# Performance work log

Hardware: AMD Instinct MI355X
Metric: run time of the kernel (lower is better)

## Reference

```python
import jax, jax.numpy as jnp
import numpy as np

DIM = 1024
NUM_HEADS = 16
HEAD_DIM = DIM // NUM_HEADS
EPS = 1e-6


def setup_inputs() -> dict:
    key = jax.random.key(0)
    ks = jax.random.split(key, 9)
    B, S = 4, 4096
    std = 1.0 / np.sqrt(DIM)
    inp = {
        "x": jax.random.normal(ks[0], (B, S, DIM), dtype=jnp.float32),
        "attention_mask": jnp.ones((B, S), dtype=jnp.float32),
        "Wq": jax.random.normal(ks[1], (DIM, DIM), dtype=jnp.float32) * std,
        "bq": jnp.zeros((DIM,), dtype=jnp.float32),
        "Wk": jax.random.normal(ks[2], (DIM, DIM), dtype=jnp.float32) * std,
        "bk": jnp.zeros((DIM,), dtype=jnp.float32),
        "Wv": jax.random.normal(ks[3], (DIM, DIM), dtype=jnp.float32) * std,
        "bv": jnp.zeros((DIM,), dtype=jnp.float32),
        "Wo": jax.random.normal(ks[4], (DIM, DIM), dtype=jnp.float32) * std,
        "bo": jnp.zeros((DIM,), dtype=jnp.float32),
    }
    return inp


def _phi(x):
    # ELU + 1 feature map (positive-valued kernel features)
    return jax.nn.elu(x) + 1.0


def reference(x, attention_mask, Wq, bq, Wk, bk, Wv, bv, Wo, bo):
    B, S, _ = x.shape
    H, D = NUM_HEADS, HEAD_DIM
    q = (x @ Wq.T + bq).reshape(B, S, H, D)
    k = (x @ Wk.T + bk).reshape(B, S, H, D)
    v = (x @ Wv.T + bv).reshape(B, S, H, D)
    q = _phi(q)
    k = _phi(k)
    m = attention_mask[:, :, None, None]
    k = k * m
    v = v * m
    # kv state: [B, H, D, D]
    kv = jnp.einsum("bshd,bshm->bhdm", k, v)
    qkv = jnp.einsum("bshd,bhdm->bshm", q, kv)
    k_sum = k.sum(axis=1)  # [B, H, D]
    normalizer = jnp.einsum("bshd,bhd->bsh", q, k_sum) + EPS
    out = (qkv / normalizer[..., None]).reshape(B, S, DIM)
    return out @ Wo.T + bo
```

## Files before the change

kernel.cpp:

```cpp
#include <hip/hip_runtime.h>

typedef unsigned short u16;
typedef float f32x4 __attribute__((ext_vector_type(4)));
typedef __bf16 bf16x8 __attribute__((ext_vector_type(8)));
typedef unsigned short us8 __attribute__((ext_vector_type(8)));

#define EPS_ 1e-6f

__device__ __forceinline__ u16 f2bf(float f) {
    unsigned u = __float_as_uint(f);
    u += 0x7FFFu + ((u >> 16) & 1u);
    return (u16)(u >> 16);
}
__device__ __forceinline__ float bf2f(u16 h) {
    return __uint_as_float(((unsigned)h) << 16);
}
__device__ __forceinline__ void gload_lds16(const void* g, void* l) {
    __builtin_amdgcn_global_load_lds(
        (const __attribute__((address_space(1))) void*)g,
        (__attribute__((address_space(3))) void*)l, 16, 0, 0);
}

__global__ __launch_bounds__(256) void f32_to_bf16_kernel(
    const float* __restrict__ src, u16* __restrict__ dst, int n4)
{
    int i = blockIdx.x * 256 + threadIdx.x;
    if (i >= n4) return;
    float4 f = ((const float4*)src)[i];
    ushort4 o;
    o.x = f2bf(f.x); o.y = f2bf(f.y); o.z = f2bf(f.z); o.w = f2bf(f.w);
    ((ushort4*)dst)[i] = o;
}


__device__ __forceinline__ void stage_half(
    const u16* __restrict__ src, int K, int kbase, char* slot, int tid)
{
    const int w = tid >> 6, l = tid & 63;
    #pragma unroll
    for (int j = 0; j < 2; ++j) {
        int c16 = j * 512 + w * 64 + l;
        int row = c16 >> 2;
        int sl  = c16 & 3;
        int ksrc = kbase + ((sl ^ ((row >> 1) & 3)) << 3);
        gload_lds16(src + (size_t)row * K + ksrc, slot + j * 8192 + w * 1024);
    }
}

#define BARRIER()  asm volatile("s_barrier" ::: "memory")
#define VMCNT4()   asm volatile("s_waitcnt vmcnt(4)" ::: "memory")

#define LOADA8(base) \
    af0 = *(const bf16x8*)((base) + aoff + 0);    \
    af1 = *(const bf16x8*)((base) + aoff + 1024); \
    af2 = *(const bf16x8*)((base) + aoff + 2048); \
    af3 = *(const bf16x8*)((base) + aoff + 3072); \
    af4 = *(const bf16x8*)((base) + aoff + 4096); \
    af5 = *(const bf16x8*)((base) + aoff + 5120); \
    af6 = *(const bf16x8*)((base) + aoff + 6144); \
    af7 = *(const bf16x8*)((base) + aoff + 7168);

#define LOADB4(base) \
    bf0 = *(const bf16x8*)((base) + boff + 0);    \
    bf1 = *(const bf16x8*)((base) + boff + 1024); \
    bf2 = *(const bf16x8*)((base) + boff + 2048); \
    bf3 = *(const bf16x8*)((base) + boff + 3072);

#define MFMA1(M_, N_, AF_, BF_) \
    acc[M_][N_] = __builtin_amdgcn_mfma_f32_16x16x32_bf16(BF_, AF_, acc[M_][N_], 0, 0, 0)

#define MFMA_ROW(M_, AF_) \
    MFMA1(M_, 0, AF_, bf0); MFMA1(M_, 1, AF_, bf1); \
    MFMA1(M_, 2, AF_, bf2); MFMA1(M_, 3, AF_, bf3);

#define MFMA_HALF() do { \
    __builtin_amdgcn_s_setprio(1); \
    MFMA_ROW(0, af0); MFMA_ROW(1, af1); MFMA_ROW(2, af2); MFMA_ROW(3, af3); \
    MFMA_ROW(4, af4); MFMA_ROW(5, af5); MFMA_ROW(6, af6); MFMA_ROW(7, af7); \
    __builtin_amdgcn_s_setprio(0); \
} while (0)

template<int MODE>
__global__ __launch_bounds__(512, 2) void gemm8p(
    const u16* __restrict__ A, const u16* __restrict__ B,
    const float* __restrict__ bias,
    u16* __restrict__ oq, u16* __restrict__ ok, u16* __restrict__ ov,
    float* __restrict__ outf, int M, int N, int K)
{
    extern __shared__ char lds[];
    const int tid  = threadIdx.x;
    const int lane = tid & 63;
    const int wv   = tid >> 6;
    const int wm   = wv >> 2;
    const int wn   = wv & 3;
    const int NT = K >> 6;

    int bx, by;
    {
        const int gx = gridDim.x;
        int wg  = blockIdx.y * gx + blockIdx.x;
        int cpx = (gx * gridDim.y) >> 3;
        int swz = (wg & 7) * cpx + (wg >> 3);
        bx = swz % gx; by = swz / gx;
    }

    const u16* Ab = A + (size_t)by * 256 * K;
    const u16* Bb = B + (size_t)bx * 256 * K;

    const int i  = lane & 15, g = lane >> 4;
    const int fo = ((g ^ ((i >> 1) & 3)) << 4);
    const int aoff = (wm * 128 + i) * 64 + fo;
    const int boff = (wn * 64 + i) * 64 + fo;

    f32x4 acc[8][4];
    #pragma unroll
    for (int m = 0; m < 8; ++m)
        #pragma unroll
        for (int n = 0; n < 4; ++n) {
            acc[m][n][0] = 0.f; acc[m][n][1] = 0.f;
            acc[m][n][2] = 0.f; acc[m][n][3] = 0.f;
        }

    stage_half(Ab, K, 0,  lds + 0,             tid);
    stage_half(Bb, K, 0,  lds + 16384,         tid);
    stage_half(Ab, K, 32, lds + 32768,         tid);
    stage_half(Bb, K, 32, lds + 49152,         tid);
    stage_half(Ab, K, 64, lds + 65536 + 0,     tid);
    stage_half(Bb, K, 64, lds + 65536 + 16384, tid);

    for (int t = 0; t < NT; ++t) {
        char* cb = lds + ((t & 1) << 16);
        char* nb = lds + (((t + 1) & 1) << 16);
        const int t1 = (t + 1 < NT) ? t + 1 : NT - 1;
        const int t2 = (t + 2 < NT) ? t + 2 : NT - 1;

        VMCNT4();
        BARRIER();

        bf16x8 af0, af1, af2, af3, af4, af5, af6, af7, bf0, bf1, bf2, bf3;

        stage_half(Ab, K, t1 * 64 + 32, nb + 32768, tid);
        stage_half(Bb, K, t1 * 64 + 32, nb + 49152, tid);

        LOADA8(cb);
        LOADB4(cb + 16384);
        MFMA_HALF();

        BARRIER();

        stage_half(Ab, K, t2 * 64, cb + 0,     tid);
        stage_half(Bb, K, t2 * 64, cb + 16384, tid);

        LOADA8(cb + 32768);
        LOADB4(cb + 49152);
        MFMA_HALF();
    }
    asm volatile("s_waitcnt vmcnt(0)" ::: "memory");

    const int rowg0 = by * 256 + wm * 128;
    const int colg0 = bx * 256 + wn * 64;

    if (MODE == 1) {
        const int which = colg0 >> 10;
        u16* dst = (which == 0) ? oq : ((which == 1) ? ok : ov);
        const bool dophi = (which < 2);
        const int cbo = colg0 & 1023;
        float4 bs[4];
        #pragma unroll
        for (int n = 0; n < 4; ++n)
            bs[n] = *(const float4*)(bias + colg0 + n * 16 + g * 4);
        #pragma unroll
        for (int m = 0; m < 8; ++m) {
            int row = rowg0 + m * 16 + i;
            #pragma unroll
            for (int n = 0; n < 4; ++n) {
                float v0 = acc[m][n][0] + bs[n].x;
                float v1 = acc[m][n][1] + bs[n].y;
                float v2 = acc[m][n][2] + bs[n].z;
                float v3 = acc[m][n][3] + bs[n].w;
                if (dophi) {
                    v0 = (v0 > 0.f) ? (v0 + 1.f) : __expf(v0);
                    v1 = (v1 > 0.f) ? (v1 + 1.f) : __expf(v1);
                    v2 = (v2 > 0.f) ? (v2 + 1.f) : __expf(v2);
                    v3 = (v3 > 0.f) ? (v3 + 1.f) : __expf(v3);
                }
                ushort4 o;
                o.x = f2bf(v0); o.y = f2bf(v1); o.z = f2bf(v2); o.w = f2bf(v3);
                *(ushort4*)(dst + (size_t)row * 1024 + cbo + n * 16 + g * 4) = o;
            }
        }
    } else {
        float4 bs[4];
        #pragma unroll
        for (int n = 0; n < 4; ++n)
            bs[n] = *(const float4*)(bias + colg0 + n * 16 + g * 4);
        #pragma unroll
        for (int m = 0; m < 8; ++m) {
            int row = rowg0 + m * 16 + i;
            #pragma unroll
            for (int n = 0; n < 4; ++n) {
                float4 o;
                o.x = acc[m][n][0] + bs[n].x;
                o.y = acc[m][n][1] + bs[n].y;
                o.z = acc[m][n][2] + bs[n].z;
                o.w = acc[m][n][3] + bs[n].w;
                *(float4*)(outf + (size_t)row * N + colg0 + n * 16 + g * 4) = o;
            }
        }
    }
}

__global__ __launch_bounds__(256) void kv_partial(
    const u16* __restrict__ kbf, const u16* __restrict__ vbf,
    const float* __restrict__ mask, float* __restrict__ kvp, float* __restrict__ ksp)
{
    const int bh = blockIdx.x, ch = blockIdx.y;
    const int b = bh >> 4, h = bh & 15;
    const int tid = threadIdx.x;
    __shared__ __align__(16) float ks[32][64];
    __shared__ __align__(16) float vs[32][64];
    const int dg = tid >> 4, mg = tid & 15;
    float acc[4][4] = {};
    float ksa[4] = {};
    const int s0 = ch * 256;
    const int lr = tid >> 3, lc = (tid & 7) * 8;
    for (int sb = 0; sb < 256; sb += 32) {
        {
            size_t grow = (size_t)b * 4096 + (s0 + sb + lr);
            float mm = mask[grow];
            size_t off = (grow << 10) + (h << 6) + lc;
            us8 ku = __builtin_bit_cast(us8, *(const bf16x8*)(kbf + off));
            us8 vu = __builtin_bit_cast(us8, *(const bf16x8*)(vbf + off));
            #pragma unroll
            for (int j = 0; j < 8; ++j) {
                ks[lr][lc + j] = bf2f(ku[j]) * mm;
                vs[lr][lc + j] = bf2f(vu[j]) * mm;
            }
        }
        __syncthreads();
        #pragma unroll
        for (int ss = 0; ss < 32; ++ss) {
            float4 k4 = *(const float4*)&ks[ss][dg << 2];
            float4 v4 = *(const float4*)&vs[ss][mg << 2];
            float ka[4] = {k4.x, k4.y, k4.z, k4.w};
            float va[4] = {v4.x, v4.y, v4.z, v4.w};
            #pragma unroll
            for (int di = 0; di < 4; ++di) {
                ksa[di] += ka[di];
                #pragma unroll
                for (int mi = 0; mi < 4; ++mi) acc[di][mi] += ka[di] * va[mi];
            }
        }
        __syncthreads();
    }
    float* o = kvp + (((size_t)ch * 64 + bh) << 12);
    #pragma unroll
    for (int di = 0; di < 4; ++di)
        #pragma unroll
        for (int mi = 0; mi < 4; ++mi)
            o[(dg * 4 + di) * 64 + (mg * 4 + mi)] = acc[di][mi];
    if (mg == 0) {
        float* os = ksp + (((size_t)ch * 64 + bh) << 6);
        #pragma unroll
        for (int di = 0; di < 4; ++di) os[dg * 4 + di] = ksa[di];
    }
}

__global__ __launch_bounds__(256) void kv_reduce(
    const float* __restrict__ kvp, const float* __restrict__ ksp,
    u16* __restrict__ kvTbf, u16* __restrict__ ksumbf)
{
    const int bh = blockIdx.x, tid = threadIdx.x;
    for (int idx = tid; idx < 4096; idx += 256) {
        float s = 0.f;
        #pragma unroll
        for (int c = 0; c < 16; ++c) s += kvp[(((size_t)c * 64 + bh) << 12) + idx];
        int d = idx >> 6, m = idx & 63;
        kvTbf[((size_t)bh << 12) + (m << 6) + d] = f2bf(s);
    }
    if (tid < 64) {
        float s = 0.f;
        #pragma unroll
        for (int c = 0; c < 16; ++c) s += ksp[(((size_t)c * 64 + bh) << 6) + tid];
        ksumbf[(bh << 6) + tid] = f2bf(s);
    }
}

__global__ __launch_bounds__(256) void attn_kernel(
    const u16* __restrict__ qbf, const u16* __restrict__ kvTbf,
    const u16* __restrict__ ksumbf, u16* __restrict__ attnbf)
{
    const int bh = blockIdx.x;
    const int b = bh >> 4, h = bh & 15;
    const int tid = threadIdx.x, lane = tid & 63, wv = tid >> 6;
    __shared__ __align__(16) u16 kvs[64 * 64];
    __shared__ __align__(16) u16 kss[64];

    {
        const uint4* src = (const uint4*)(kvTbf + ((size_t)bh << 12));
        for (int u = tid; u < 512; u += 256) {
            uint4 d4 = src[u];
            int m = u >> 3, slot = u & 7;
            *(uint4*)((char*)kvs + m * 128 + ((slot ^ (m & 7)) << 4)) = d4;
        }
        if (tid < 32)
            ((unsigned*)kss)[tid] = ((const unsigned*)(ksumbf + ((size_t)bh << 6)))[tid];
    }
    __syncthreads();

    bf16x8 bfr[2][4], bnf[2];
    #pragma unroll
    for (int kk = 0; kk < 2; ++kk) {
        int kslot = kk * 4 + (lane >> 4);
        #pragma unroll
        for (int n = 0; n < 4; ++n) {
            int m = n * 16 + (lane & 15);
            bfr[kk][n] = *(const bf16x8*)((const char*)kvs + m * 128 +
                                          ((kslot ^ (m & 7)) << 4));
        }
        #pragma unroll
        for (int i2 = 0; i2 < 8; ++i2) bnf[kk][i2] = (__bf16)0.0f;
        if ((lane & 15) == 0)
            bnf[kk] = *(const bf16x8*)((const char*)kss + (kslot << 4));
    }

    const int sbase = blockIdx.y * 256 + wv * 16;
    for (int it = 0; it < 4; ++it) {
        const int st = sbase + it * 64;
        f32x4 acc[4], nacc;
        #pragma unroll
        for (int n = 0; n < 4; ++n) {
            acc[n][0] = 0.f; acc[n][1] = 0.f; acc[n][2] = 0.f; acc[n][3] = 0.f;
        }
        nacc[0] = 0.f; nacc[1] = 0.f; nacc[2] = 0.f; nacc[3] = 0.f;
        #pragma unroll
        for (int kk = 0; kk < 2; ++kk) {
            size_t goff = (((size_t)(b * 4096 + st + (lane & 15))) << 10) +
                          (h << 6) + kk * 32 + ((lane >> 4) << 3);
            bf16x8 af = *(const bf16x8*)(qbf + goff);
            #pragma unroll
            for (int n = 0; n < 4; ++n)
                acc[n] = __builtin_amdgcn_mfma_f32_16x16x32_bf16(af, bfr[kk][n], acc[n], 0, 0, 0);
            nacc = __builtin_amdgcn_mfma_f32_16x16x32_bf16(af, bnf[kk], nacc, 0, 0, 0);
        }
        float inv[4];
        #pragma unroll
        for (int j = 0; j < 4; ++j) {
            float nj = __shfl(nacc[j], lane & 48);
            inv[j] = 1.0f / (nj + EPS_);
        }
        #pragma unroll
        for (int n = 0; n < 4; ++n)
            #pragma unroll
            for (int j = 0; j < 4; ++j) {
                int row = st + ((lane >> 4) << 2) + j;
                attnbf[(((size_t)(b * 4096 + row)) << 10) + (h << 6) + n * 16 + (lane & 15)]
                    = f2bf(acc[n][j] * inv[j]);
            }
    }
}

extern "C" void kernel_launch(void* const* d_in, const int* in_sizes, int n_in,
                              void* d_out, int out_size, void* d_ws, size_t ws_size,
                              hipStream_t stream) {
    const float* x    = (const float*)d_in[0];
    const float* mask = (const float*)d_in[1];
    const float* Wq   = (const float*)d_in[2];
    const float* bq   = (const float*)d_in[3];
    const float* Wk   = (const float*)d_in[4];
    const float* bk   = (const float*)d_in[5];
    const float* Wv   = (const float*)d_in[6];
    const float* bv   = (const float*)d_in[7];
    const float* Wo   = (const float*)d_in[8];
    const float* bo   = (const float*)d_in[9];
    float* out = (float*)d_out;

    if (ws_size < 142606336u) return;

    char* ws = (char*)d_ws;
    u16*   xbf    = (u16*)ws;
    u16*   wqkvbf = (u16*)(ws + 33554432);
    float* bcat   = (float*)(ws + 39845888);
    u16*   qbf    = (u16*)(ws + 41943040);
    u16*   kbf    = qbf + 16777216;
    u16*   vbf    = kbf + 16777216;
    u16*   attnbf = kbf;
    float* kvp    = (float*)ws;
    float* ksp    = (float*)(ws + 16777216);
    u16*   kvTbf  = (u16*)(ws + 17039360);
    u16*   ksumbf = (u16*)(ws + 17563648);
    u16*   wobf   = (u16*)(ws + 20971520);

    f32_to_bf16_kernel<<<16384, 256, 0, stream>>>(x,  xbf,  16777216 / 4);
    f32_to_bf16_kernel<<<1024,  256, 0, stream>>>(Wq, wqkvbf,           1048576 / 4);
    f32_to_bf16_kernel<<<1024,  256, 0, stream>>>(Wk, wqkvbf + 1048576, 1048576 / 4);
    f32_to_bf16_kernel<<<1024,  256, 0, stream>>>(Wv, wqkvbf + 2097152, 1048576 / 4);
    hipMemcpyAsync(bcat,        bq, 4096, hipMemcpyDeviceToDevice, stream);
    hipMemcpyAsync(bcat + 1024, bk, 4096, hipMemcpyDeviceToDevice, stream);
    hipMemcpyAsync(bcat + 2048, bv, 4096, hipMemcpyDeviceToDevice, stream);

    gemm8p<1><<<dim3(12, 64), 512, 131072, stream>>>(
        xbf, wqkvbf, bcat, qbf, kbf, vbf, nullptr, 16384, 3072, 1024);

    f32_to_bf16_kernel<<<1024, 256, 0, stream>>>(Wo, wobf, 1048576 / 4);

    kv_partial<<<dim3(64, 16), 256, 0, stream>>>(kbf, vbf, mask, kvp, ksp);
    kv_reduce<<<64, 256, 0, stream>>>(kvp, ksp, kvTbf, ksumbf);

    attn_kernel<<<dim3(64, 16), 256, 0, stream>>>(qbf, kvTbf, ksumbf, attnbf);

    gemm8p<0><<<dim3(4, 64), 512, 131072, stream>>>(
        attnbf, wobf, bo, nullptr, nullptr, nullptr, out, 16384, 1024, 1024);
}
```

Before: 247.2 us.

## Restructure GEMM main loop to full-tile double buffering with interleaved LDS reads

```diff
diff --git a/kernel.cpp b/kernel.cpp
--- a/kernel.cpp
+++ b/kernel.cpp
@@ -48,37 +48,19 @@
 }
 
 #define BARRIER()  asm volatile("s_barrier" ::: "memory")
-#define VMCNT4()   asm volatile("s_waitcnt vmcnt(4)" ::: "memory")
-
-#define LOADA8(base) \
-    af0 = *(const bf16x8*)((base) + aoff + 0);    \
-    af1 = *(const bf16x8*)((base) + aoff + 1024); \
-    af2 = *(const bf16x8*)((base) + aoff + 2048); \
-    af3 = *(const bf16x8*)((base) + aoff + 3072); \
-    af4 = *(const bf16x8*)((base) + aoff + 4096); \
-    af5 = *(const bf16x8*)((base) + aoff + 5120); \
-    af6 = *(const bf16x8*)((base) + aoff + 6144); \
-    af7 = *(const bf16x8*)((base) + aoff + 7168);
-
-#define LOADB4(base) \
-    bf0 = *(const bf16x8*)((base) + boff + 0);    \
-    bf1 = *(const bf16x8*)((base) + boff + 1024); \
-    bf2 = *(const bf16x8*)((base) + boff + 2048); \
-    bf3 = *(const bf16x8*)((base) + boff + 3072);
+#define VMCNT0()   asm volatile("s_waitcnt vmcnt(0)" ::: "memory")
 
 #define MFMA1(M_, N_, AF_, BF_) \
     acc[M_][N_] = __builtin_amdgcn_mfma_f32_16x16x32_bf16(BF_, AF_, acc[M_][N_], 0, 0, 0)
 
-#define MFMA_ROW(M_, AF_) \
-    MFMA1(M_, 0, AF_, bf0); MFMA1(M_, 1, AF_, bf1); \
-    MFMA1(M_, 2, AF_, bf2); MFMA1(M_, 3, AF_, bf3);
-
-#define MFMA_HALF() do { \
-    __builtin_amdgcn_s_setprio(1); \
-    MFMA_ROW(0, af0); MFMA_ROW(1, af1); MFMA_ROW(2, af2); MFMA_ROW(3, af3); \
-    MFMA_ROW(4, af4); MFMA_ROW(5, af5); MFMA_ROW(6, af6); MFMA_ROW(7, af7); \
-    __builtin_amdgcn_s_setprio(0); \
+#define QUAD(M0, A0_, A1_, A2_, A3_, B0_, B1_, B2_, B3_) do { \
+    MFMA1(M0+0, 0, A0_, B0_); MFMA1(M0+0, 1, A0_, B1_); MFMA1(M0+0, 2, A0_, B2_); MFMA1(M0+0, 3, A0_, B3_); \
+    MFMA1(M0+1, 0, A1_, B0_); MFMA1(M0+1, 1, A1_, B1_); MFMA1(M0+1, 2, A1_, B2_); MFMA1(M0+1, 3, A1_, B3_); \
+    MFMA1(M0+2, 0, A2_, B0_); MFMA1(M0+2, 1, A2_, B1_); MFMA1(M0+2, 2, A2_, B2_); MFMA1(M0+2, 3, A2_, B3_); \
+    MFMA1(M0+3, 0, A3_, B0_); MFMA1(M0+3, 1, A3_, B1_); MFMA1(M0+3, 2, A3_, B2_); MFMA1(M0+3, 3, A3_, B3_); \
 } while (0)
+
+#define RD(dst_, base_, off_) dst_ = *(const bf16x8*)((base_) + (off_))
 
 template<int MODE>
 __global__ __launch_bounds__(512, 2) void gemm8p(
@@ -121,41 +103,50 @@
             acc[m][n][2] = 0.f; acc[m][n][3] = 0.f;
         }
 
-    stage_half(Ab, K, 0,  lds + 0,             tid);
-    stage_half(Bb, K, 0,  lds + 16384,         tid);
-    stage_half(Ab, K, 32, lds + 32768,         tid);
-    stage_half(Bb, K, 32, lds + 49152,         tid);
-    stage_half(Ab, K, 64, lds + 65536 + 0,     tid);
-    stage_half(Bb, K, 64, lds + 65536 + 16384, tid);
+    stage_half(Ab, K, 0,  lds + 0,     tid);
+    stage_half(Bb, K, 0,  lds + 16384, tid);
+    stage_half(Ab, K, 32, lds + 32768, tid);
+    stage_half(Bb, K, 32, lds + 49152, tid);
 
     for (int t = 0; t < NT; ++t) {
         char* cb = lds + ((t & 1) << 16);
         char* nb = lds + (((t + 1) & 1) << 16);
         const int t1 = (t + 1 < NT) ? t + 1 : NT - 1;
-        const int t2 = (t + 2 < NT) ? t + 2 : NT - 1;
-
-        VMCNT4();
+
+        VMCNT0();
         BARRIER();
 
-        bf16x8 af0, af1, af2, af3, af4, af5, af6, af7, bf0, bf1, bf2, bf3;
-
+        stage_half(Ab, K, t1 * 64,      nb + 0,     tid);
+        stage_half(Bb, K, t1 * 64,      nb + 16384, tid);
         stage_half(Ab, K, t1 * 64 + 32, nb + 32768, tid);
         stage_half(Bb, K, t1 * 64 + 32, nb + 49152, tid);
 
-        LOADA8(cb);
-        LOADB4(cb + 16384);
-        MFMA_HALF();
-
-        BARRIER();
-
-        stage_half(Ab, K, t2 * 64, cb + 0,     tid);
-        stage_half(Bb, K, t2 * 64, cb + 16384, tid);
-
-        LOADA8(cb + 32768);
-        LOADB4(cb + 49152);
-        MFMA_HALF();
-    }
-    asm volatile("s_waitcnt vmcnt(0)" ::: "memory");
+        bf16x8 aL0, aL1, aL2, aL3, aH0, aH1, aH2, aH3, b00, b01, b02, b03;
+        bf16x8 cL0, cL1, cL2, cL3, cH0, cH1, cH2, cH3, b10, b11, b12, b13;
+
+        RD(aL0, cb, aoff + 0);    RD(aL1, cb, aoff + 1024);
+        RD(aL2, cb, aoff + 2048); RD(aL3, cb, aoff + 3072);
+        RD(b00, cb + 16384, boff + 0);    RD(b01, cb + 16384, boff + 1024);
+        RD(b02, cb + 16384, boff + 2048); RD(b03, cb + 16384, boff + 3072);
+        RD(aH0, cb, aoff + 4096); RD(aH1, cb, aoff + 5120);
+        RD(aH2, cb, aoff + 6144); RD(aH3, cb, aoff + 7168);
+
+        QUAD(0, aL0, aL1, aL2, aL3, b00, b01, b02, b03);
+
+        RD(cL0, cb + 32768, aoff + 0);    RD(cL1, cb + 32768, aoff + 1024);
+        RD(cL2, cb + 32768, aoff + 2048); RD(cL3, cb + 32768, aoff + 3072);
+        RD(b10, cb + 49152, boff + 0);    RD(b11, cb + 49152, boff + 1024);
+        RD(b12, cb + 49152, boff + 2048); RD(b13, cb + 49152, boff + 3072);
+
+        QUAD(4, aH0, aH1, aH2, aH3, b00, b01, b02, b03);
+
+        RD(cH0, cb + 32768, aoff + 4096); RD(cH1, cb + 32768, aoff + 5120);
+        RD(cH2, cb + 32768, aoff + 6144); RD(cH3, cb + 32768, aoff + 7168);
+
+        QUAD(0, cL0, cL1, cL2, cL3, b10, b11, b12, b13);
+        QUAD(4, cH0, cH1, cH2, cH3, b10, b11, b12, b13);
+    }
+    VMCNT0();
 
     const int rowg0 = by * 256 + wm * 128;
     const int colg0 = bx * 256 + wn * 64;
```

Result: no change. 251.0 us (+1.5%).
